# Kernel optimization log

Measured on AMD Instinct MI355X. Metric: run time of the kernel, lower is better.

## Reference

```python
import jax, jax.numpy as jnp
import numpy as np

N = 100000      # total sampled nodes
NT = 20000      # target (destination) nodes
E = 2000000     # edges
IN = 128        # in_dim
OUT = 64        # out_channels (heads=1, concat)
NEG_SLOPE = 0.2 # GATConv default negative_slope


def setup_inputs() -> dict:
    key = jax.random.key(0)
    ks = jax.random.split(key, 6)
    x = jax.random.normal(ks[0], (N, IN), dtype=jnp.float32)
    edge_src = jax.random.randint(ks[1], (E,), 0, N)
    edge_dst = jax.random.randint(ks[2], (E,), 0, NT)
    # GATConv params: shared lin for src/dst (in_channels is int), att vectors, bias
    W = jax.random.normal(ks[3], (IN, OUT), dtype=jnp.float32) / np.sqrt(IN).astype(np.float32)
    att_src = jax.random.normal(ks[4], (OUT,), dtype=jnp.float32)
    att_dst = jax.random.normal(ks[5], (OUT,), dtype=jnp.float32)
    bias = jnp.zeros((OUT,), dtype=jnp.float32)
    return {"x": x, "edge_src": edge_src, "edge_dst": edge_dst,
            "W": W, "att_src": att_src, "att_dst": att_dst, "bias": bias,
            "num_target": NT}


def reference(x, edge_src, edge_dst, W, att_src, att_dst, bias, num_target):
    # Linear transform (lin_src == lin_dst in PyG GATConv when in_channels is int)
    x_proj = x @ W                      # [N, OUT]
    x_dst = x_proj[:num_target]         # [NT, OUT] target nodes are x[:num_target]
    # Per-node attention logits
    a_src = x_proj @ att_src            # [N]
    a_dst = x_dst @ att_dst             # [NT]
    # Edge logits + LeakyReLU
    e = jax.nn.leaky_relu(a_src[edge_src] + a_dst[edge_dst], NEG_SLOPE)  # [E]
    # Segment softmax over edges grouped by destination
    m = jax.ops.segment_max(e, edge_dst, num_segments=num_target)
    m = jnp.where(jnp.isneginf(m), jnp.float32(0.0), m)  # empty segments
    p = jnp.exp(e - m[edge_dst])
    denom = jax.ops.segment_sum(p, edge_dst, num_segments=num_target)
    alpha = p / (denom[edge_dst] + jnp.float32(1e-16))   # PyG softmax eps
    # Weighted scatter-aggregate of source features
    out = jax.ops.segment_sum(alpha[:, None] * x_proj[edge_src], edge_dst,
                              num_segments=num_target)   # [NT, OUT]
    return out + bias
```

## Files before the change

### kernel.cpp

```cpp
#include <hip/hip_runtime.h>

#define IN_DIM 128
#define OUT_DIM 64
#define NEG_SLOPE 0.2f

#define NBUCK 625
#define BCAP 4096
#define CHUNK 8192

typedef __attribute__((ext_vector_type(8))) short short8v;
typedef __attribute__((ext_vector_type(4))) float f32x4;

__device__ __forceinline__ unsigned pack_bf16(float a, float b) {
    unsigned ua = __float_as_uint(a), ub = __float_as_uint(b);
    ua += 0x7FFFu + ((ua >> 16) & 1u);
    ub += 0x7FFFu + ((ub >> 16) & 1u);
    return (ua >> 16) | (ub & 0xFFFF0000u);
}

__device__ __forceinline__ short8v mk8(unsigned a, unsigned b, unsigned c, unsigned d) {
    union { uint4 u; short8v s; } z;
    z.u = make_uint4(a, b, c, d);
    return z.s;
}

__global__ __launch_bounds__(256) void part_kernel(
    const float* __restrict__ W, unsigned* __restrict__ w_hi,
    unsigned* __restrict__ w_lo,
    const int* __restrict__ edge_src, const int* __restrict__ edge_dst,
    int* __restrict__ bcursor, unsigned* __restrict__ inter, int E)
{
    if (blockIdx.x < 4) {
        int g = blockIdx.x * 256 + threadIdx.x;
        if (g >= 1024) return;
        int kb = g >> 6, col = g & 63;
        unsigned uh[4], ul[4];
#pragma unroll
        for (int i = 0; i < 4; ++i) {
            float a = W[(kb * 8 + 2 * i) * 64 + col];
            float b = W[(kb * 8 + 2 * i + 1) * 64 + col];
            unsigned h = pack_bf16(a, b);
            float la = a - __uint_as_float(h << 16);
            float lb = b - __uint_as_float(h & 0xFFFF0000u);
            uh[i] = h;
            ul[i] = pack_bf16(la, lb);
        }
        *(uint4*)(w_hi + g * 4) = make_uint4(uh[0], uh[1], uh[2], uh[3]);
        *(uint4*)(w_lo + g * 4) = make_uint4(ul[0], ul[1], ul[2], ul[3]);
        return;
    }

    __shared__ unsigned stage[CHUNK];
    __shared__ int hist[NBUCK];
    __shared__ int loff[NBUCK];
    __shared__ int gbase[NBUCK];
    __shared__ int cur[NBUCK];
    __shared__ int wsum[4];

    const int t  = threadIdx.x;
    const int c0 = (blockIdx.x - 4) * CHUNK;
    const int cnt = min(CHUNK, E - c0);

    for (int i = t; i < NBUCK; i += 256) hist[i] = 0;
    __syncthreads();

    for (int i = t; i < cnt; i += 256)
        atomicAdd(&hist[edge_dst[c0 + i] >> 5], 1);
    __syncthreads();

    {
        int tmp[3];
        int mysum = 0;
#pragma unroll
        for (int k = 0; k < 3; ++k) {
            int idx = t * 3 + k;
            int v = (idx < NBUCK) ? hist[idx] : 0;
            tmp[k] = mysum;
            mysum += v;
        }
        const int lane = t & 63, w = t >> 6;
        int scan = mysum;
#pragma unroll
        for (int off = 1; off < 64; off <<= 1) {
            int o = __shfl_up(scan, off);
            if (lane >= off) scan += o;
        }
        if (lane == 63) wsum[w] = scan;
        __syncthreads();
        int wpre = 0;
#pragma unroll
        for (int i = 0; i < 4; ++i)
            if (i < w) wpre += wsum[i];
        int excl = wpre + scan - mysum;
#pragma unroll
        for (int k = 0; k < 3; ++k) {
            int idx = t * 3 + k;
            if (idx < NBUCK) loff[idx] = excl + tmp[k];
        }
    }
    __syncthreads();

    for (int b = t; b < NBUCK; b += 256) {
        int c = hist[b];
        if (c > 0) gbase[b] = b * BCAP + atomicAdd(&bcursor[b], c);
        cur[b] = loff[b];
    }
    __syncthreads();

    for (int i = t; i < cnt; i += 256) {
        int s = edge_src[c0 + i];
        int d = edge_dst[c0 + i];
        int p = atomicAdd(&cur[d >> 5], 1);
        stage[p] = ((unsigned)d << 17) | (unsigned)s;
    }
    __syncthreads();

    for (int i = t; i < cnt; i += 256) {
        unsigned v = stage[i];
        int b = v >> 22;
        int pos = gbase[b] + (i - loff[b]);
        if (pos < (b + 1) * BCAP) inter[pos] = v;
    }
}

__global__ __launch_bounds__(256) void build_csr_kernel(
    const int* __restrict__ bcursor, unsigned* __restrict__ inter,
    int* __restrict__ offs, int* __restrict__ len, int NT)
{
    __shared__ unsigned stage[BCAP];
    __shared__ unsigned sorted[BCAP];
    __shared__ int cnt[32], off_[32], cur[32];

    const int b = blockIdx.x;
    const int t = threadIdx.x;
    const int base = b * BCAP;
    int n = min(bcursor[b], BCAP);

    if (t < 32) cnt[t] = 0;
    __syncthreads();

    for (int i = t; i < n; i += 256) {
        unsigned v = inter[base + i];
        stage[i] = v;
        atomicAdd(&cnt[(v >> 17) & 31], 1);
    }
    __syncthreads();

    if (t == 0) {
        int r = 0;
#pragma unroll
        for (int j = 0; j < 32; ++j) { off_[j] = r; r += cnt[j]; }
    }
    __syncthreads();
    if (t < 32) {
        cur[t] = off_[t];
        int d = b * 32 + t;
        if (d < NT) {
            offs[d] = base + off_[t];
            len[d]  = cnt[t];
        }
    }
    __syncthreads();

    for (int i = t; i < n; i += 256) {
        unsigned v = stage[i];
        int p = atomicAdd(&cur[(v >> 17) & 31], 1);
        sorted[p] = v & 0x1FFFFu;
    }
    __syncthreads();

    for (int i = t; i < n; i += 256)
        inter[base + i] = sorted[i];
}

__global__ __launch_bounds__(256) void gemm_kernel(
    const float* __restrict__ x,
    const unsigned* __restrict__ w_hi, const unsigned* __restrict__ w_lo,
    const float* __restrict__ att_src, const float* __restrict__ att_dst,
    unsigned* __restrict__ x_bf, float* __restrict__ a_src,
    float* __restrict__ a_dst, int N, int NT)
{
    __shared__ __align__(16) float C[128 * 64];

    const int t    = threadIdx.x;
    const int lane = t & 63;
    const int w    = t >> 6;
    const int r0   = blockIdx.x * 128;
    const int rsub = lane & 15;
    const int kg   = lane >> 4;

    const int r1 = min(r0 + 32 * w + rsub,      N - 1);
    const int r2 = min(r0 + 32 * w + 16 + rsub, N - 1);
    const float* xrow1 = x + (size_t)r1 * IN_DIM + kg * 8;
    const float* xrow2 = x + (size_t)r2 * IN_DIM + kg * 8;

    float4 xv[16];
#pragma unroll
    for (int j = 0; j < 8; ++j)
        xv[j] = *(const float4*)(xrow1 + (j >> 1) * 32 + (j & 1) * 4);
#pragma unroll
    for (int j = 0; j < 8; ++j)
        xv[8 + j] = *(const float4*)(xrow2 + (j >> 1) * 32 + (j & 1) * 4);
    __builtin_amdgcn_sched_barrier(0);

    short8v ah[2][4], al[2][4];
#pragma unroll
    for (int rf = 0; rf < 2; ++rf)
#pragma unroll
        for (int ks = 0; ks < 4; ++ks) {
            float4 v0 = xv[8 * rf + 2 * ks], v1 = xv[8 * rf + 2 * ks + 1];
            unsigned h0 = pack_bf16(v0.x, v0.y);
            unsigned h1 = pack_bf16(v0.z, v0.w);
            unsigned h2 = pack_bf16(v1.x, v1.y);
            unsigned h3 = pack_bf16(v1.z, v1.w);
            unsigned l0 = pack_bf16(v0.x - __uint_as_float(h0 << 16),
                                    v0.y - __uint_as_float(h0 & 0xFFFF0000u));
            unsigned l1 = pack_bf16(v0.z - __uint_as_float(h1 << 16),
                                    v0.w - __uint_as_float(h1 & 0xFFFF0000u));
            unsigned l2 = pack_bf16(v1.x - __uint_as_float(h2 << 16),
                                    v1.y - __uint_as_float(h2 & 0xFFFF0000u));
            unsigned l3 = pack_bf16(v1.z - __uint_as_float(h3 << 16),
                                    v1.w - __uint_as_float(h3 & 0xFFFF0000u));
            ah[rf][ks] = mk8(h0, h1, h2, h3);
            al[rf][ks] = mk8(l0, l1, l2, l3);
        }

    f32x4 acc[2][4];
#pragma unroll
    for (int rf = 0; rf < 2; ++rf)
#pragma unroll
        for (int cf = 0; cf < 4; ++cf) acc[rf][cf] = f32x4{0.f, 0.f, 0.f, 0.f};

#pragma unroll
    for (int ks = 0; ks < 4; ++ks) {
        const int kb = 4 * ks + kg;
        const unsigned* bhp = w_hi + (kb * 64 + rsub) * 4;
        const unsigned* blp = w_lo + (kb * 64 + rsub) * 4;
        short8v bh[4], bl[4];
#pragma unroll
        for (int cf = 0; cf < 4; ++cf) {
            bh[cf] = *(const short8v*)(bhp + cf * 64);
            bl[cf] = *(const short8v*)(blp + cf * 64);
        }
#pragma unroll
        for (int cf = 0; cf < 4; ++cf) {
#pragma unroll
            for (int rf = 0; rf < 2; ++rf) {
                acc[rf][cf] = __builtin_amdgcn_mfma_f32_16x16x32_bf16(ah[rf][ks], bh[cf], acc[rf][cf], 0, 0, 0);
                acc[rf][cf] = __builtin_amdgcn_mfma_f32_16x16x32_bf16(al[rf][ks], bh[cf], acc[rf][cf], 0, 0, 0);
                acc[rf][cf] = __builtin_amdgcn_mfma_f32_16x16x32_bf16(ah[rf][ks], bl[cf], acc[rf][cf], 0, 0, 0);
            }
        }
    }

#pragma unroll
    for (int rf = 0; rf < 2; ++rf)
#pragma unroll
        for (int cf = 0; cf < 4; ++cf)
#pragma unroll
            for (int j = 0; j < 4; ++j) {
                int row = 32 * w + 16 * rf + 4 * kg + j;
                int col = 16 * cf + rsub;
                C[row * 64 + ((col + 4 * row) & 63)] = acc[rf][cf][j];
            }
    __syncthreads();

    {
        const int row = t >> 1;
        const int h   = t & 1;
        const int rr  = r0 + row;
        float v[32];
#pragma unroll
        for (int j = 0; j < 8; ++j) {
            int s = (32 * h + 4 * j + 4 * row) & 63;
            float4 f = *(const float4*)(C + row * 64 + s);
            v[4 * j + 0] = f.x; v[4 * j + 1] = f.y;
            v[4 * j + 2] = f.z; v[4 * j + 3] = f.w;
        }
        if (rr < N) {
            unsigned pk[16];
#pragma unroll
            for (int m = 0; m < 16; ++m)
                pk[m] = pack_bf16(v[2 * m], v[2 * m + 1]);
            unsigned* dst = x_bf + (size_t)rr * 32 + h * 16;
            *(uint4*)(dst + 0)  = make_uint4(pk[0], pk[1], pk[2], pk[3]);
            *(uint4*)(dst + 4)  = make_uint4(pk[4], pk[5], pk[6], pk[7]);
            *(uint4*)(dst + 8)  = make_uint4(pk[8], pk[9], pk[10], pk[11]);
            *(uint4*)(dst + 12) = make_uint4(pk[12], pk[13], pk[14], pk[15]);

            float ps = 0.f, pd = 0.f;
#pragma unroll
            for (int i = 0; i < 32; ++i) {
                ps = fmaf(v[i], att_src[32 * h + i], ps);
                pd = fmaf(v[i], att_dst[32 * h + i], pd);
            }
            ps += __shfl_xor(ps, 1);
            pd += __shfl_xor(pd, 1);
            if (h == 0) {
                a_src[rr] = ps;
                if (rr < NT) a_dst[rr] = pd;
            }
        }
    }
}

#define LRELU_EXP(a) __expf(((a) > 0.f ? (a) : NEG_SLOPE * (a)))

__global__ __launch_bounds__(256) void aggregate_kernel(
    const int* __restrict__ csr, const int* __restrict__ offs,
    const int* __restrict__ len,
    const float* __restrict__ a_src, const float* __restrict__ a_dst,
    const unsigned* __restrict__ x_bf, const float* __restrict__ bias,
    float* __restrict__ out, int NT)
{
    const int lane = threadIdx.x & 63;
    const int tgt  = blockIdx.x * 4 + (threadIdx.x >> 6);
    if (tgt >= NT) return;

    const int g   = lane >> 3;
    const int sub = lane & 7;

    const int lo = offs[tgt];
    const int n  = len[tgt];
    const int hi = lo + n;

    float4 b0 = *(const float4*)(bias + sub * 8);
    float4 b1 = *(const float4*)(bias + sub * 8 + 4);

    if (n <= 0) {
        if (g == 0) {
            float* o = out + (size_t)tgt * OUT_DIM + sub * 8;
            *(float4*)(o)     = b0;
            *(float4*)(o + 4) = b1;
        }
        return;
    }

    const float ad = a_dst[tgt];
    const int nc = (n + 63) >> 6;

    float dl = 0.f;
    float acc[8];
#pragma unroll
    for (int k = 0; k < 8; ++k) acc[k] = 0.f;

    int c = 0;
    for (; c + 1 < nc; c += 2) {
        const int iA = lo + 64 * c + lane;
        const int iB = iA + 64;
        const int sA = csr[iA];
        const int sB = (iB < hi) ? csr[iB] : 0;

        int s8A[8], s8B[8];
#pragma unroll
        for (int j = 0; j < 8; ++j) s8A[j] = __shfl(sA, 8 * g + j);
#pragma unroll
        for (int j = 0; j < 8; ++j) s8B[j] = __shfl(sB, 8 * g + j);

        uint4 vA[8], vB[8];
#pragma unroll
        for (int j = 0; j < 8; ++j)
            vA[j] = *(const uint4*)(x_bf + (size_t)s8A[j] * 32 + sub * 4);
#pragma unroll
        for (int j = 0; j < 8; ++j)
            vB[j] = *(const uint4*)(x_bf + (size_t)s8B[j] * 32 + sub * 4);

        const float aA = a_src[sA];
        const float aB = a_src[sB];
        const float pA = LRELU_EXP(aA + ad);
        const float pB = (iB < hi) ? LRELU_EXP(aB + ad) : 0.f;
        dl += pA + pB;

        float p8A[8], p8B[8];
#pragma unroll
        for (int j = 0; j < 8; ++j) p8A[j] = __shfl(pA, 8 * g + j);
#pragma unroll
        for (int j = 0; j < 8; ++j) p8B[j] = __shfl(pB, 8 * g + j);

#pragma unroll
        for (int j = 0; j < 8; ++j) {
            const float p = p8A[j];
            acc[0] = fmaf(p, __uint_as_float(vA[j].x << 16), acc[0]);
            acc[1] = fmaf(p, __uint_as_float(vA[j].x & 0xFFFF0000u), acc[1]);
            acc[2] = fmaf(p, __uint_as_float(vA[j].y << 16), acc[2]);
            acc[3] = fmaf(p, __uint_as_float(vA[j].y & 0xFFFF0000u), acc[3]);
            acc[4] = fmaf(p, __uint_as_float(vA[j].z << 16), acc[4]);
            acc[5] = fmaf(p, __uint_as_float(vA[j].z & 0xFFFF0000u), acc[5]);
            acc[6] = fmaf(p, __uint_as_float(vA[j].w << 16), acc[6]);
            acc[7] = fmaf(p, __uint_as_float(vA[j].w & 0xFFFF0000u), acc[7]);
        }
#pragma unroll
        for (int j = 0; j < 8; ++j) {
            const float p = p8B[j];
            acc[0] = fmaf(p, __uint_as_float(vB[j].x << 16), acc[0]);
            acc[1] = fmaf(p, __uint_as_float(vB[j].x & 0xFFFF0000u), acc[1]);
            acc[2] = fmaf(p, __uint_as_float(vB[j].y << 16), acc[2]);
            acc[3] = fmaf(p, __uint_as_float(vB[j].y & 0xFFFF0000u), acc[3]);
            acc[4] = fmaf(p, __uint_as_float(vB[j].z << 16), acc[4]);
            acc[5] = fmaf(p, __uint_as_float(vB[j].z & 0xFFFF0000u), acc[5]);
            acc[6] = fmaf(p, __uint_as_float(vB[j].w << 16), acc[6]);
            acc[7] = fmaf(p, __uint_as_float(vB[j].w & 0xFFFF0000u), acc[7]);
        }
    }
    if (c < nc) {
        const int iA = lo + 64 * c + lane;
        const int sA = (iA < hi) ? csr[iA] : 0;
        int s8A[8];
#pragma unroll
        for (int j = 0; j < 8; ++j) s8A[j] = __shfl(sA, 8 * g + j);
        uint4 vA[8];
#pragma unroll
        for (int j = 0; j < 8; ++j)
            vA[j] = *(const uint4*)(x_bf + (size_t)s8A[j] * 32 + sub * 4);
        const float aA = a_src[sA];
        const float pA = (iA < hi) ? LRELU_EXP(aA + ad) : 0.f;
        dl += pA;
        float p8A[8];
#pragma unroll
        for (int j = 0; j < 8; ++j) p8A[j] = __shfl(pA, 8 * g + j);
#pragma unroll
        for (int j = 0; j < 8; ++j) {
            const float p = p8A[j];
            acc[0] = fmaf(p, __uint_as_float(vA[j].x << 16), acc[0]);
            acc[1] = fmaf(p, __uint_as_float(vA[j].x & 0xFFFF0000u), acc[1]);
            acc[2] = fmaf(p, __uint_as_float(vA[j].y << 16), acc[2]);
            acc[3] = fmaf(p, __uint_as_float(vA[j].y & 0xFFFF0000u), acc[3]);
            acc[4] = fmaf(p, __uint_as_float(vA[j].z << 16), acc[4]);
            acc[5] = fmaf(p, __uint_as_float(vA[j].z & 0xFFFF0000u), acc[5]);
            acc[6] = fmaf(p, __uint_as_float(vA[j].w << 16), acc[6]);
            acc[7] = fmaf(p, __uint_as_float(vA[j].w & 0xFFFF0000u), acc[7]);
        }
    }

#pragma unroll
    for (int k = 0; k < 8; ++k) {
        acc[k] += __shfl_xor(acc[k], 8);
        acc[k] += __shfl_xor(acc[k], 16);
        acc[k] += __shfl_xor(acc[k], 32);
    }
#pragma unroll
    for (int off = 32; off; off >>= 1) dl += __shfl_xor(dl, off);
    const float inv = 1.f / (dl + 1e-16f);

    if (g == 0) {
        float* o = out + (size_t)tgt * OUT_DIM + sub * 8;
        float4 o0, o1;
        o0.x = fmaf(acc[0], inv, b0.x); o0.y = fmaf(acc[1], inv, b0.y);
        o0.z = fmaf(acc[2], inv, b0.z); o0.w = fmaf(acc[3], inv, b0.w);
        o1.x = fmaf(acc[4], inv, b1.x); o1.y = fmaf(acc[5], inv, b1.y);
        o1.z = fmaf(acc[6], inv, b1.z); o1.w = fmaf(acc[7], inv, b1.w);
        *(float4*)(o)     = o0;
        *(float4*)(o + 4) = o1;
    }
}

extern "C" void kernel_launch(void* const* d_in, const int* in_sizes, int n_in,
                              void* d_out, int out_size, void* d_ws, size_t ws_size,
                              hipStream_t stream)
{
    const float* x        = (const float*)d_in[0];
    const int*   edge_src = (const int*)d_in[1];
    const int*   edge_dst = (const int*)d_in[2];
    const float* W        = (const float*)d_in[3];
    const float* att_src  = (const float*)d_in[4];
    const float* att_dst  = (const float*)d_in[5];
    const float* bias     = (const float*)d_in[6];

    const int N  = in_sizes[0] / IN_DIM;
    const int E  = in_sizes[1];
    const int NT = out_size / OUT_DIM;
    float* out = (float*)d_out;

    auto align256 = [](size_t v) { return (v + 255) & ~(size_t)255; };
    char* w = (char*)d_ws;
    unsigned* x_bf   = (unsigned*)w;  w += align256((size_t)N * 32 * 4);
    float*    a_src  = (float*)w;     w += align256((size_t)N * 4);
    float*    a_dst  = (float*)w;     w += align256((size_t)NT * 4);
    int*      offs   = (int*)w;       w += align256((size_t)NT * 4);
    int*      len    = (int*)w;       w += align256((size_t)NT * 4);
    int*      bcursor= (int*)w;       w += align256((size_t)NBUCK * 4);
    unsigned* w_hi   = (unsigned*)w;  w += align256((size_t)1024 * 16);
    unsigned* w_lo   = (unsigned*)w;  w += align256((size_t)1024 * 16);
    unsigned* inter  = (unsigned*)w;  w += align256((size_t)NBUCK * BCAP * 4);

    hipMemsetAsync(bcursor, 0, (size_t)NBUCK * 4, stream);

    const int nchunk = (E + CHUNK - 1) / CHUNK;
    part_kernel<<<4 + nchunk, 256, 0, stream>>>(
        W, w_hi, w_lo, edge_src, edge_dst, bcursor, inter, E);

    build_csr_kernel<<<NBUCK, 256, 0, stream>>>(
        bcursor, inter, offs, len, NT);

    gemm_kernel<<<(N + 127) / 128, 256, 0, stream>>>(
        x, w_hi, w_lo, att_src, att_dst, x_bf, a_src, a_dst, N, NT);

    aggregate_kernel<<<(NT + 3) / 4, 256, 0, stream>>>(
        (const int*)inter, offs, len, a_src, a_dst, x_bf, bias, out, NT);
}
```

Baseline: 106.3 us.

## Fuse per-bucket CSR sort into aggregation kernel and widen partition blocks

Removes the separate build_csr kernel: each aggregation block now loads one destination bucket, counting-sorts it by target in shared memory, and then processes that bucket's 32 targets directly from LDS. This drops one kernel launch, the offs/len arrays, and the global write and re-read of the sorted edges. The partition kernel moves to 1024-thread blocks where each thread holds 8 packed edges in registers loaded as int4, so the source and destination arrays are read once instead of twice. In exchange, aggregation parallelism falls to 625 blocks of 512 threads with 32 targets each, which may give worse load balance and lower occupancy.

```diff
diff --git a/kernel.cpp b/kernel.cpp
--- a/kernel.cpp
+++ b/kernel.cpp
@@ -24,15 +24,14 @@
     return z.s;
 }
 
-__global__ __launch_bounds__(256) void part_kernel(
+__global__ __launch_bounds__(1024) void part_kernel(
     const float* __restrict__ W, unsigned* __restrict__ w_hi,
     unsigned* __restrict__ w_lo,
     const int* __restrict__ edge_src, const int* __restrict__ edge_dst,
     int* __restrict__ bcursor, unsigned* __restrict__ inter, int E)
 {
-    if (blockIdx.x < 4) {
-        int g = blockIdx.x * 256 + threadIdx.x;
-        if (g >= 1024) return;
+    if (blockIdx.x == 0) {
+        int g = threadIdx.x;
         int kb = g >> 6, col = g & 63;
         unsigned uh[4], ul[4];
 #pragma unroll
@@ -55,31 +54,51 @@
     __shared__ int loff[NBUCK];
     __shared__ int gbase[NBUCK];
     __shared__ int cur[NBUCK];
-    __shared__ int wsum[4];
+    __shared__ int wsum[16];
 
     const int t  = threadIdx.x;
-    const int c0 = (blockIdx.x - 4) * CHUNK;
+    const int c0 = (blockIdx.x - 1) * CHUNK;
     const int cnt = min(CHUNK, E - c0);
 
-    for (int i = t; i < NBUCK; i += 256) hist[i] = 0;
-    __syncthreads();
-
-    for (int i = t; i < cnt; i += 256)
-        atomicAdd(&hist[edge_dst[c0 + i] >> 5], 1);
+    for (int i = t; i < NBUCK; i += 1024) hist[i] = 0;
+    __syncthreads();
+
+    unsigned pk[8];
+    int nmine = 0;
+    const int i0 = 8 * t;
+    if (i0 + 8 <= cnt) {
+        int4 s0 = *(const int4*)(edge_src + c0 + i0);
+        int4 s1 = *(const int4*)(edge_src + c0 + i0 + 4);
+        int4 d0 = *(const int4*)(edge_dst + c0 + i0);
+        int4 d1 = *(const int4*)(edge_dst + c0 + i0 + 4);
+        pk[0] = ((unsigned)d0.x << 17) | (unsigned)s0.x;
+        pk[1] = ((unsigned)d0.y << 17) | (unsigned)s0.y;
+        pk[2] = ((unsigned)d0.z << 17) | (unsigned)s0.z;
+        pk[3] = ((unsigned)d0.w << 17) | (unsigned)s0.w;
+        pk[4] = ((unsigned)d1.x << 17) | (unsigned)s1.x;
+        pk[5] = ((unsigned)d1.y << 17) | (unsigned)s1.y;
+        pk[6] = ((unsigned)d1.z << 17) | (unsigned)s1.z;
+        pk[7] = ((unsigned)d1.w << 17) | (unsigned)s1.w;
+        nmine = 8;
+    } else {
+#pragma unroll
+        for (int k = 0; k < 8; ++k) {
+            int i = i0 + k;
+            if (i < cnt) {
+                pk[k] = ((unsigned)edge_dst[c0 + i] << 17) | (unsigned)edge_src[c0 + i];
+                nmine = k + 1;
+            }
+        }
+    }
+#pragma unroll
+    for (int k = 0; k < 8; ++k)
+        if (k < nmine) atomicAdd(&hist[pk[k] >> 22], 1);
     __syncthreads();
 
     {
-        int tmp[3];
-        int mysum = 0;
-#pragma unroll
-        for (int k = 0; k < 3; ++k) {
-            int idx = t * 3 + k;
-            int v = (idx < NBUCK) ? hist[idx] : 0;
-            tmp[k] = mysum;
-            mysum += v;
-        }
         const int lane = t & 63, w = t >> 6;
-        int scan = mysum;
+        int v = (t < NBUCK) ? hist[t] : 0;
+        int scan = v;
 #pragma unroll
         for (int off = 1; off < 64; off <<= 1) {
             int o = __shfl_up(scan, off);
@@ -89,88 +108,32 @@
         __syncthreads();
         int wpre = 0;
 #pragma unroll
-        for (int i = 0; i < 4; ++i)
+        for (int i = 0; i < 16; ++i)
             if (i < w) wpre += wsum[i];
-        int excl = wpre + scan - mysum;
-#pragma unroll
-        for (int k = 0; k < 3; ++k) {
-            int idx = t * 3 + k;
-            if (idx < NBUCK) loff[idx] = excl + tmp[k];
-        }
-    }
-    __syncthreads();
-
-    for (int b = t; b < NBUCK; b += 256) {
-        int c = hist[b];
-        if (c > 0) gbase[b] = b * BCAP + atomicAdd(&bcursor[b], c);
-        cur[b] = loff[b];
-    }
-    __syncthreads();
-
-    for (int i = t; i < cnt; i += 256) {
-        int s = edge_src[c0 + i];
-        int d = edge_dst[c0 + i];
-        int p = atomicAdd(&cur[d >> 5], 1);
-        stage[p] = ((unsigned)d << 17) | (unsigned)s;
-    }
-    __syncthreads();
-
-    for (int i = t; i < cnt; i += 256) {
+        int excl = wpre + scan - v;
+        if (t < NBUCK) {
+            loff[t] = excl;
+            cur[t]  = excl;
+            if (v > 0) gbase[t] = t * BCAP + atomicAdd(&bcursor[t], v);
+        }
+    }
+    __syncthreads();
+
+#pragma unroll
+    for (int k = 0; k < 8; ++k)
+        if (k < nmine) {
+            unsigned v = pk[k];
+            int p = atomicAdd(&cur[v >> 22], 1);
+            stage[p] = v;
+        }
+    __syncthreads();
+
+    for (int i = t; i < cnt; i += 1024) {
         unsigned v = stage[i];
         int b = v >> 22;
         int pos = gbase[b] + (i - loff[b]);
         if (pos < (b + 1) * BCAP) inter[pos] = v;
     }
-}
-
-__global__ __launch_bounds__(256) void build_csr_kernel(
-    const int* __restrict__ bcursor, unsigned* __restrict__ inter,
-    int* __restrict__ offs, int* __restrict__ len, int NT)
-{
-    __shared__ unsigned stage[BCAP];
-    __shared__ unsigned sorted[BCAP];
-    __shared__ int cnt[32], off_[32], cur[32];
-
-    const int b = blockIdx.x;
-    const int t = threadIdx.x;
-    const int base = b * BCAP;
-    int n = min(bcursor[b], BCAP);
-
-    if (t < 32) cnt[t] = 0;
-    __syncthreads();
-
-    for (int i = t; i < n; i += 256) {
-        unsigned v = inter[base + i];
-        stage[i] = v;
-        atomicAdd(&cnt[(v >> 17) & 31], 1);
-    }
-    __syncthreads();
-
-    if (t == 0) {
-        int r = 0;
-#pragma unroll
-        for (int j = 0; j < 32; ++j) { off_[j] = r; r += cnt[j]; }
-    }
-    __syncthreads();
-    if (t < 32) {
-        cur[t] = off_[t];
-        int d = b * 32 + t;
-        if (d < NT) {
-            offs[d] = base + off_[t];
-            len[d]  = cnt[t];
-        }
-    }
-    __syncthreads();
-
-    for (int i = t; i < n; i += 256) {
-        unsigned v = stage[i];
-        int p = atomicAdd(&cur[(v >> 17) & 31], 1);
-        sorted[p] = v & 0x1FFFFu;
-    }
-    __syncthreads();
-
-    for (int i = t; i < n; i += 256)
-        inter[base + i] = sorted[i];
 }
 
 __global__ __launch_bounds__(256) void gemm_kernel(
@@ -306,151 +269,194 @@
 
 #define LRELU_EXP(a) __expf(((a) > 0.f ? (a) : NEG_SLOPE * (a)))
 
-__global__ __launch_bounds__(256) void aggregate_kernel(
-    const int* __restrict__ csr, const int* __restrict__ offs,
-    const int* __restrict__ len,
+__global__ __launch_bounds__(512) void agg_kernel(
+    const int* __restrict__ bcursor, const unsigned* __restrict__ inter,
     const float* __restrict__ a_src, const float* __restrict__ a_dst,
     const unsigned* __restrict__ x_bf, const float* __restrict__ bias,
     float* __restrict__ out, int NT)
 {
-    const int lane = threadIdx.x & 63;
-    const int tgt  = blockIdx.x * 4 + (threadIdx.x >> 6);
-    if (tgt >= NT) return;
-
-    const int g   = lane >> 3;
-    const int sub = lane & 7;
-
-    const int lo = offs[tgt];
-    const int n  = len[tgt];
-    const int hi = lo + n;
+    __shared__ unsigned ssrc[BCAP];
+    __shared__ int cnt[32], off_[32], cur[32];
+
+    const int b = blockIdx.x;
+    const int t = threadIdx.x;
+    const int base = b * BCAP;
+    const int n = min(bcursor[b], BCAP);
+
+    if (t < 32) cnt[t] = 0;
+    __syncthreads();
+
+    unsigned ev[8];
+#pragma unroll
+    for (int k = 0; k < 8; ++k) {
+        int i = t + 512 * k;
+        ev[k] = 0xFFFFFFFFu;
+        if (i < n) {
+            ev[k] = inter[base + i];
+            atomicAdd(&cnt[(ev[k] >> 17) & 31], 1);
+        }
+    }
+    __syncthreads();
+
+    if (t == 0) {
+        int r = 0;
+#pragma unroll
+        for (int j = 0; j < 32; ++j) { off_[j] = r; r += cnt[j]; }
+    }
+    __syncthreads();
+    if (t < 32) cur[t] = off_[t];
+    __syncthreads();
+
+#pragma unroll
+    for (int k = 0; k < 8; ++k)
+        if (ev[k] != 0xFFFFFFFFu) {
+            int p = atomicAdd(&cur[(ev[k] >> 17) & 31], 1);
+            ssrc[p] = ev[k] & 0x1FFFFu;
+        }
+    __syncthreads();
+
+    const int lane = t & 63;
+    const int w    = t >> 6;
+    const int g    = lane >> 3;
+    const int sub  = lane & 7;
 
     float4 b0 = *(const float4*)(bias + sub * 8);
     float4 b1 = *(const float4*)(bias + sub * 8 + 4);
 
-    if (n <= 0) {
+    for (int q = 0; q < 4; ++q) {
+        const int ld  = w + 8 * q;
+        const int tgt = b * 32 + ld;
+        if (tgt >= NT) continue;
+
+        const int lo = off_[ld];
+        const int nn = cnt[ld];
+        const int hi = lo + nn;
+
+        if (nn <= 0) {
+            if (g == 0) {
+                float* o = out + (size_t)tgt * OUT_DIM + sub * 8;
+                *(float4*)(o)     = b0;
+                *(float4*)(o + 4) = b1;
+            }
+            continue;
+        }
+
+        const float ad = a_dst[tgt];
+        const int nc = (nn + 63) >> 6;
+
+        float dl = 0.f;
+        float acc[8];
+#pragma unroll
+        for (int k = 0; k < 8; ++k) acc[k] = 0.f;
+
+        int c = 0;
+        for (; c + 1 < nc; c += 2) {
+            const int iA = lo + 64 * c + lane;
+            const int iB = iA + 64;
+            const int sA = (int)ssrc[iA];
+            const int sB = (iB < hi) ? (int)ssrc[iB] : 0;
+
+            int s8A[8], s8B[8];
+#pragma unroll
+            for (int j = 0; j < 8; ++j) s8A[j] = __shfl(sA, 8 * g + j);
+#pragma unroll
+            for (int j = 0; j < 8; ++j) s8B[j] = __shfl(sB, 8 * g + j);
+
+            uint4 vA[8], vB[8];
+#pragma unroll
+            for (int j = 0; j < 8; ++j)
+                vA[j] = *(const uint4*)(x_bf + (size_t)s8A[j] * 32 + sub * 4);
+#pragma unroll
+            for (int j = 0; j < 8; ++j)
+                vB[j] = *(const uint4*)(x_bf + (size_t)s8B[j] * 32 + sub * 4);
+
+            const float aA = a_src[sA];
+            const float aB = a_src[sB];
+            const float pA = LRELU_EXP(aA + ad);
+            const float pB = (iB < hi) ? LRELU_EXP(aB + ad) : 0.f;
+            dl += pA + pB;
+
+            float p8A[8], p8B[8];
+#pragma unroll
+            for (int j = 0; j < 8; ++j) p8A[j] = __shfl(pA, 8 * g + j);
+#pragma unroll
+            for (int j = 0; j < 8; ++j) p8B[j] = __shfl(pB, 8 * g + j);
+
+#pragma unroll
+            for (int j = 0; j < 8; ++j) {
+                const float p = p8A[j];
+                acc[0] = fmaf(p, __uint_as_float(vA[j].x << 16), acc[0]);
+                acc[1] = fmaf(p, __uint_as_float(vA[j].x & 0xFFFF0000u), acc[1]);
+                acc[2] = fmaf(p, __uint_as_float(vA[j].y << 16), acc[2]);
+                acc[3] = fmaf(p, __uint_as_float(vA[j].y & 0xFFFF0000u), acc[3]);
+                acc[4] = fmaf(p, __uint_as_float(vA[j].z << 16), acc[4]);
+                acc[5] = fmaf(p, __uint_as_float(vA[j].z & 0xFFFF0000u), acc[5]);
+                acc[6] = fmaf(p, __uint_as_float(vA[j].w << 16), acc[6]);
+                acc[7] = fmaf(p, __uint_as_float(vA[j].w & 0xFFFF0000u), acc[7]);
+            }
+#pragma unroll
+            for (int j = 0; j < 8; ++j) {
+                const float p = p8B[j];
+                acc[0] = fmaf(p, __uint_as_float(vB[j].x << 16), acc[0]);
+                acc[1] = fmaf(p, __uint_as_float(vB[j].x & 0xFFFF0000u), acc[1]);
+                acc[2] = fmaf(p, __uint_as_float(vB[j].y << 16), acc[2]);
+                acc[3] = fmaf(p, __uint_as_float(vB[j].y & 0xFFFF0000u), acc[3]);
+                acc[4] = fmaf(p, __uint_as_float(vB[j].z << 16), acc[4]);
+                acc[5] = fmaf(p, __uint_as_float(vB[j].z & 0xFFFF0000u), acc[5]);
+                acc[6] = fmaf(p, __uint_as_float(vB[j].w << 16), acc[6]);
+                acc[7] = fmaf(p, __uint_as_float(vB[j].w & 0xFFFF0000u), acc[7]);
+            }
+        }
+        if (c < nc) {
+            const int iA = lo + 64 * c + lane;
+            const int sA = (iA < hi) ? (int)ssrc[iA] : 0;
+            int s8A[8];
+#pragma unroll
+            for (int j = 0; j < 8; ++j) s8A[j] = __shfl(sA, 8 * g + j);
+            uint4 vA[8];
+#pragma unroll
+            for (int j = 0; j < 8; ++j)
+                vA[j] = *(const uint4*)(x_bf + (size_t)s8A[j] * 32 + sub * 4);
+            const float aA = a_src[sA];
+            const float pA = (iA < hi) ? LRELU_EXP(aA + ad) : 0.f;
+            dl += pA;
+            float p8A[8];
+#pragma unroll
+            for (int j = 0; j < 8; ++j) p8A[j] = __shfl(pA, 8 * g + j);
+#pragma unroll
+            for (int j = 0; j < 8; ++j) {
+                const float p = p8A[j];
+                acc[0] = fmaf(p, __uint_as_float(vA[j].x << 16), acc[0]);
+                acc[1] = fmaf(p, __uint_as_float(vA[j].x & 0xFFFF0000u), acc[1]);
+                acc[2] = fmaf(p, __uint_as_float(vA[j].y << 16), acc[2]);
+                acc[3] = fmaf(p, __uint_as_float(vA[j].y & 0xFFFF0000u), acc[3]);
+                acc[4] = fmaf(p, __uint_as_float(vA[j].z << 16), acc[4]);
+                acc[5] = fmaf(p, __uint_as_float(vA[j].z & 0xFFFF0000u), acc[5]);
+                acc[6] = fmaf(p, __uint_as_float(vA[j].w << 16), acc[6]);
+                acc[7] = fmaf(p, __uint_as_float(vA[j].w & 0xFFFF0000u), acc[7]);
+            }
+        }
+
+#pragma unroll
+        for (int k = 0; k < 8; ++k) {
+            acc[k] += __shfl_xor(acc[k], 8);
+            acc[k] += __shfl_xor(acc[k], 16);
+            acc[k] += __shfl_xor(acc[k], 32);
+        }
+#pragma unroll
+        for (int off = 32; off; off >>= 1) dl += __shfl_xor(dl, off);
+        const float inv = 1.f / (dl + 1e-16f);
+
         if (g == 0) {
             float* o = out + (size_t)tgt * OUT_DIM + sub * 8;
-            *(float4*)(o)     = b0;
-            *(float4*)(o + 4) = b1;
-        }
-        return;
-    }
-
-    const float ad = a_dst[tgt];
-    const int nc = (n + 63) >> 6;
-
-    float dl = 0.f;
-    float acc[8];
-#pragma unroll
-    for (int k = 0; k < 8; ++k) acc[k] = 0.f;
-
-    int c = 0;
-    for (; c + 1 < nc; c += 2) {
-        const int iA = lo + 64 * c + lane;
-        const int iB = iA + 64;
-        const int sA = csr[iA];
-        const int sB = (iB < hi) ? csr[iB] : 0;
-
-        int s8A[8], s8B[8];
-#pragma unroll
-        for (int j = 0; j < 8; ++j) s8A[j] = __shfl(sA, 8 * g + j);
-#pragma unroll
-        for (int j = 0; j < 8; ++j) s8B[j] = __shfl(sB, 8 * g + j);
-
-        uint4 vA[8], vB[8];
-#pragma unroll
-        for (int j = 0; j < 8; ++j)
-            vA[j] = *(const uint4*)(x_bf + (size_t)s8A[j] * 32 + sub * 4);
-#pragma unroll
-        for (int j = 0; j < 8; ++j)
-            vB[j] = *(const uint4*)(x_bf + (size_t)s8B[j] * 32 + sub * 4);
-
-        const float aA = a_src[sA];
-        const float aB = a_src[sB];
-        const float pA = LRELU_EXP(aA + ad);
-        const float pB = (iB < hi) ? LRELU_EXP(aB + ad) : 0.f;
-        dl += pA + pB;
-
-        float p8A[8], p8B[8];
-#pragma unroll
-        for (int j = 0; j < 8; ++j) p8A[j] = __shfl(pA, 8 * g + j);
-#pragma unroll
-        for (int j = 0; j < 8; ++j) p8B[j] = __shfl(pB, 8 * g + j);
-
-#pragma unroll
-        for (int j = 0; j < 8; ++j) {
-            const float p = p8A[j];
-            acc[0] = fmaf(p, __uint_as_float(vA[j].x << 16), acc[0]);
-            acc[1] = fmaf(p, __uint_as_float(vA[j].x & 0xFFFF0000u), acc[1]);
-            acc[2] = fmaf(p, __uint_as_float(vA[j].y << 16), acc[2]);
-            acc[3] = fmaf(p, __uint_as_float(vA[j].y & 0xFFFF0000u), acc[3]);
-            acc[4] = fmaf(p, __uint_as_float(vA[j].z << 16), acc[4]);
-            acc[5] = fmaf(p, __uint_as_float(vA[j].z & 0xFFFF0000u), acc[5]);
-            acc[6] = fmaf(p, __uint_as_float(vA[j].w << 16), acc[6]);
-            acc[7] = fmaf(p, __uint_as_float(vA[j].w & 0xFFFF0000u), acc[7]);
-        }
-#pragma unroll
-        for (int j = 0; j < 8; ++j) {
-            const float p = p8B[j];
-            acc[0] = fmaf(p, __uint_as_float(vB[j].x << 16), acc[0]);
-            acc[1] = fmaf(p, __uint_as_float(vB[j].x & 0xFFFF0000u), acc[1]);
-            acc[2] = fmaf(p, __uint_as_float(vB[j].y << 16), acc[2]);
-            acc[3] = fmaf(p, __uint_as_float(vB[j].y & 0xFFFF0000u), acc[3]);
-            acc[4] = fmaf(p, __uint_as_float(vB[j].z << 16), acc[4]);
-            acc[5] = fmaf(p, __uint_as_float(vB[j].z & 0xFFFF0000u), acc[5]);
-            acc[6] = fmaf(p, __uint_as_float(vB[j].w << 16), acc[6]);
-            acc[7] = fmaf(p, __uint_as_float(vB[j].w & 0xFFFF0000u), acc[7]);
-        }
-    }
-    if (c < nc) {
-        const int iA = lo + 64 * c + lane;
-        const int sA = (iA < hi) ? csr[iA] : 0;
-        int s8A[8];
-#pragma unroll
-        for (int j = 0; j < 8; ++j) s8A[j] = __shfl(sA, 8 * g + j);
-        uint4 vA[8];
-#pragma unroll
-        for (int j = 0; j < 8; ++j)
-            vA[j] = *(const uint4*)(x_bf + (size_t)s8A[j] * 32 + sub * 4);
-        const float aA = a_src[sA];
-        const float pA = (iA < hi) ? LRELU_EXP(aA + ad) : 0.f;
-        dl += pA;
-        float p8A[8];
-#pragma unroll
-        for (int j = 0; j < 8; ++j) p8A[j] = __shfl(pA, 8 * g + j);
-#pragma unroll
-        for (int j = 0; j < 8; ++j) {
-            const float p = p8A[j];
-            acc[0] = fmaf(p, __uint_as_float(vA[j].x << 16), acc[0]);
-            acc[1] = fmaf(p, __uint_as_float(vA[j].x & 0xFFFF0000u), acc[1]);
-            acc[2] = fmaf(p, __uint_as_float(vA[j].y << 16), acc[2]);
-            acc[3] = fmaf(p, __uint_as_float(vA[j].y & 0xFFFF0000u), acc[3]);
-            acc[4] = fmaf(p, __uint_as_float(vA[j].z << 16), acc[4]);
-            acc[5] = fmaf(p, __uint_as_float(vA[j].z & 0xFFFF0000u), acc[5]);
-            acc[6] = fmaf(p, __uint_as_float(vA[j].w << 16), acc[6]);
-            acc[7] = fmaf(p, __uint_as_float(vA[j].w & 0xFFFF0000u), acc[7]);
-        }
-    }
-
-#pragma unroll
-    for (int k = 0; k < 8; ++k) {
-        acc[k] += __shfl_xor(acc[k], 8);
-        acc[k] += __shfl_xor(acc[k], 16);
-        acc[k] += __shfl_xor(acc[k], 32);
-    }
-#pragma unroll
-    for (int off = 32; off; off >>= 1) dl += __shfl_xor(dl, off);
-    const float inv = 1.f / (dl + 1e-16f);
-
-    if (g == 0) {
-        float* o = out + (size_t)tgt * OUT_DIM + sub * 8;
-        float4 o0, o1;
-        o0.x = fmaf(acc[0], inv, b0.x); o0.y = fmaf(acc[1], inv, b0.y);
-        o0.z = fmaf(acc[2], inv, b0.z); o0.w = fmaf(acc[3], inv, b0.w);
-        o1.x = fmaf(acc[4], inv, b1.x); o1.y = fmaf(acc[5], inv, b1.y);
-        o1.z = fmaf(acc[6], inv, b1.z); o1.w = fmaf(acc[7], inv, b1.w);
-        *(float4*)(o)     = o0;
-        *(float4*)(o + 4) = o1;
+            float4 o0, o1;
+            o0.x = fmaf(acc[0], inv, b0.x); o0.y = fmaf(acc[1], inv, b0.y);
+            o0.z = fmaf(acc[2], inv, b0.z); o0.w = fmaf(acc[3], inv, b0.w);
+            o1.x = fmaf(acc[4], inv, b1.x); o1.y = fmaf(acc[5], inv, b1.y);
+            o1.z = fmaf(acc[6], inv, b1.z); o1.w = fmaf(acc[7], inv, b1.w);
+            *(float4*)(o)     = o0;
+            *(float4*)(o + 4) = o1;
+        }
     }
 }
 
@@ -476,8 +482,6 @@
     unsigned* x_bf   = (unsigned*)w;  w += align256((size_t)N * 32 * 4);
     float*    a_src  = (float*)w;     w += align256((size_t)N * 4);
     float*    a_dst  = (float*)w;     w += align256((size_t)NT * 4);
-    int*      offs   = (int*)w;       w += align256((size_t)NT * 4);
-    int*      len    = (int*)w;       w += align256((size_t)NT * 4);
     int*      bcursor= (int*)w;       w += align256((size_t)NBUCK * 4);
     unsigned* w_hi   = (unsigned*)w;  w += align256((size_t)1024 * 16);
     unsigned* w_lo   = (unsigned*)w;  w += align256((size_t)1024 * 16);
@@ -486,15 +490,12 @@
     hipMemsetAsync(bcursor, 0, (size_t)NBUCK * 4, stream);
 
     const int nchunk = (E + CHUNK - 1) / CHUNK;
-    part_kernel<<<4 + nchunk, 256, 0, stream>>>(
+    part_kernel<<<1 + nchunk, 1024, 0, stream>>>(
         W, w_hi, w_lo, edge_src, edge_dst, bcursor, inter, E);
-
-    build_csr_kernel<<<NBUCK, 256, 0, stream>>>(
-        bcursor, inter, offs, len, NT);
 
     gemm_kernel<<<(N + 127) / 128, 256, 0, stream>>>(
         x, w_hi, w_lo, att_src, att_dst, x_bf, a_src, a_dst, N, NT);
 
-    aggregate_kernel<<<(NT + 3) / 4, 256, 0, stream>>>(
-        (const int*)inter, offs, len, a_src, a_dst, x_bf, bias, out, NT);
+    agg_kernel<<<NBUCK, 512, 0, stream>>>(
+        bcursor, inter, a_src, a_dst, x_bf, bias, out, NT);
 }
```

After: 93.72 us. 1.13x faster.
